# Kernel optimization log

Measured on AMD Instinct MI355X. Metric: run time of the kernel, lower is better.

Reference implementation:

```python
import jax, jax.numpy as jnp
import numpy as np

NH, DK, DV = 8, 10, 10  # num_heads, per-head key dim, per-head value dim (dim_k=dim_v=80)


def setup_inputs() -> dict:
    key = jax.random.key(0)
    k1, k2, k3, k4, k5 = jax.random.split(key, 5)
    B, NX, NY = 64, 512, 512
    x = jax.random.normal(k1, (B, NX, 768), dtype=jnp.float32)
    y = jax.random.normal(k2, (B, NY, 283), dtype=jnp.float32)
    # nn.Linear(bias=False) weights, stored transposed as (in, out); scaled init
    Wq = jax.random.normal(k3, (768, 80), dtype=jnp.float32) * 0.02
    Wk = jax.random.normal(k4, (283, 80), dtype=jnp.float32) * 0.02
    Wv = jax.random.normal(k5, (283, 80), dtype=jnp.float32) * 0.02
    return {"x": x, "y": y, "Wq": Wq, "Wk": Wk, "Wv": Wv}


def reference(x, y, Wq, Wk, Wv):
    B, nx, _ = x.shape
    ny = y.shape[1]
    # projections -> split heads: (B, nh, seq, dhead)
    q = (x @ Wq).reshape(B, nx, NH, DK).transpose(0, 2, 1, 3)
    k = (y @ Wk).reshape(B, ny, NH, DK).transpose(0, 2, 1, 3)
    v = (y @ Wv).reshape(B, ny, NH, DV).transpose(0, 2, 1, 3)
    scale = 1.0 / np.sqrt(DK).astype(np.float32)
    dist = jax.nn.softmax(jnp.einsum("bhqd,bhkd->bhqk", q, k) * scale, axis=-1)
    att = q + jnp.einsum("bhqk,bhkd->bhqd", dist, v)  # residual add of q
    att = att.transpose(0, 2, 1, 3).reshape(B, nx, NH * DV)
    # module returns `result` = flattened attention (fc/BN stack is dead code)
    return att.reshape(B, -1)
```

## Files before the change

kernel.cpp:

```cpp
#include <hip/hip_runtime.h>
#include <stdint.h>

typedef unsigned short u16;
typedef unsigned int   u32;
typedef _Float16       f16;

typedef __attribute__((ext_vector_type(2))) _Float16 half2v;
typedef __attribute__((ext_vector_type(4))) _Float16 half4v;
typedef __attribute__((ext_vector_type(8))) _Float16 half8v;
typedef __attribute__((ext_vector_type(4))) float    floatx4;

#define NXS    512
#define NYS    512
#define NHEAD  8
#define DHEAD  10
#define DMODEL 80
#define DXK    768
#define DYK    283
#define DYKP   288

__device__ inline half2v pk2(float x, float y) {
  return __builtin_bit_cast(half2v, __builtin_amdgcn_cvt_pkrtz(x, y));
}
__device__ inline half4v cvt4(float4 v) {
  return __builtin_shufflevector(pk2(v.x, v.y), pk2(v.z, v.w), 0, 1, 2, 3);
}
__device__ inline half4v h4u32(u32 a, u32 b) {
  return __builtin_shufflevector(__builtin_bit_cast(half2v, a),
                                 __builtin_bit_cast(half2v, b), 0, 1, 2, 3);
}

__global__ __launch_bounds__(256) void w_prep(const float* __restrict__ Wq,
                                              const float* __restrict__ Wk,
                                              const float* __restrict__ Wv,
                                              f16* __restrict__ Tq,
                                              f16* __restrict__ Tk,
                                              f16* __restrict__ Tv) {
  const int idx = blockIdx.x * 256 + threadIdx.x;
  if (idx < 80 * 768) {
    const int c = idx / 768, k = idx - c * 768;
    Tq[idx] = (f16)Wq[k * 80 + c];
  }
  if (idx < 80 * 288) {
    const int c = idx / 288, k = idx - c * 288;
    float a = 0.f, b = 0.f;
    if (k < DYK) { a = Wk[k * 80 + c]; b = Wv[k * 80 + c]; }
    Tk[idx] = (f16)a;
    Tv[idx] = (f16)b;
  }
}

__global__ __launch_bounds__(256) void proj(const float* __restrict__ X,
                                            const float* __restrict__ Y,
                                            const f16* __restrict__ Wtq,
                                            const f16* __restrict__ Wtk,
                                            const f16* __restrict__ Wtv,
                                            f16* __restrict__ Qw,
                                            f16* __restrict__ Kw,
                                            f16* __restrict__ Vw) {
  const int t = threadIdx.x;
  const int wv = t >> 6, lane = t & 63, m16 = lane & 15, quad = lane >> 4;
  const int blk = blockIdx.x;

  if (blk < 512) {
    __shared__ f16 Xs[64 * 40];
    __shared__ f16 Ws[80 * 40];
    const int row0 = blk * 64;
    const int xr_r = t >> 3, xr_k = (t & 7) << 2;
    const int wi0 = t, wi1 = t + 160;

    float4 xr0, xr1;
    uint4 wr0, wr1;
    xr0 = *(const float4*)&X[(size_t)(row0 + xr_r) * DXK + xr_k];
    xr1 = *(const float4*)&X[(size_t)(row0 + xr_r + 32) * DXK + xr_k];
    if (t < 160) {
      wr0 = *(const uint4*)&Wtq[(wi0 >> 2) * DXK + (wi0 & 3) * 8];
      wr1 = *(const uint4*)&Wtq[(wi1 >> 2) * DXK + (wi1 & 3) * 8];
    }

    floatx4 acc[5];
#pragma unroll
    for (int i = 0; i < 5; ++i) acc[i] = (floatx4){0.f, 0.f, 0.f, 0.f};

    for (int s = 0; s < 24; ++s) {
      if (s) __syncthreads();
      *(half4v*)&Xs[xr_r * 40 + xr_k] = cvt4(xr0);
      *(half4v*)&Xs[(xr_r + 32) * 40 + xr_k] = cvt4(xr1);
      if (t < 160) {
        *(uint4*)&Ws[(wi0 >> 2) * 40 + (wi0 & 3) * 8] = wr0;
        *(uint4*)&Ws[(wi1 >> 2) * 40 + (wi1 & 3) * 8] = wr1;
      }
      __syncthreads();
      if (s < 23) {
        const int k0 = (s + 1) * 32;
        xr0 = *(const float4*)&X[(size_t)(row0 + xr_r) * DXK + k0 + xr_k];
        xr1 = *(const float4*)&X[(size_t)(row0 + xr_r + 32) * DXK + k0 + xr_k];
        if (t < 160) {
          wr0 = *(const uint4*)&Wtq[(wi0 >> 2) * DXK + k0 + (wi0 & 3) * 8];
          wr1 = *(const uint4*)&Wtq[(wi1 >> 2) * DXK + k0 + (wi1 & 3) * 8];
        }
      }
      const half8v a = *(const half8v*)&Xs[(wv * 16 + m16) * 40 + quad * 8];
#pragma unroll
      for (int nt = 0; nt < 5; ++nt) {
        const half8v b = *(const half8v*)&Ws[(nt * 16 + m16) * 40 + quad * 8];
        acc[nt] = __builtin_amdgcn_mfma_f32_16x16x32_f16(a, b, acc[nt], 0, 0, 0);
      }
    }
#pragma unroll
    for (int nt = 0; nt < 5; ++nt) {
      const int col = nt * 16 + m16;
#pragma unroll
      for (int p = 0; p < 4; ++p) {
        const int grow = row0 + wv * 16 + quad * 4 + p;
        Qw[(size_t)grow * DMODEL + col] = (f16)acc[nt][p];
      }
    }
  } else {
    __shared__ f16 Ys[64 * 40];
    __shared__ f16 Wks[80 * 40];
    __shared__ f16 Wvs[80 * 40];
    const int row0 = (blk - 512) * 64;
    const int wi0 = t, wi1 = t + 160;

    float yr[8];
    uint4 wk0, wk1, wv0, wv1;
#pragma unroll
    for (int i = 0; i < 8; ++i) {
      const int idx = t + 256 * i;
      const int r = idx >> 5, kk = idx & 31;
      yr[i] = Y[(size_t)(row0 + r) * DYK + kk];
    }
    if (t < 160) {
      wk0 = *(const uint4*)&Wtk[(wi0 >> 2) * DYKP + (wi0 & 3) * 8];
      wk1 = *(const uint4*)&Wtk[(wi1 >> 2) * DYKP + (wi1 & 3) * 8];
      wv0 = *(const uint4*)&Wtv[(wi0 >> 2) * DYKP + (wi0 & 3) * 8];
      wv1 = *(const uint4*)&Wtv[(wi1 >> 2) * DYKP + (wi1 & 3) * 8];
    }

    floatx4 ak[5], av[5];
#pragma unroll
    for (int i = 0; i < 5; ++i) {
      ak[i] = (floatx4){0.f, 0.f, 0.f, 0.f};
      av[i] = (floatx4){0.f, 0.f, 0.f, 0.f};
    }

    for (int s = 0; s < 9; ++s) {
      if (s) __syncthreads();
#pragma unroll
      for (int i = 0; i < 8; ++i) {
        const int idx = t + 256 * i;
        Ys[(idx >> 5) * 40 + (idx & 31)] = (f16)yr[i];
      }
      if (t < 160) {
        *(uint4*)&Wks[(wi0 >> 2) * 40 + (wi0 & 3) * 8] = wk0;
        *(uint4*)&Wks[(wi1 >> 2) * 40 + (wi1 & 3) * 8] = wk1;
        *(uint4*)&Wvs[(wi0 >> 2) * 40 + (wi0 & 3) * 8] = wv0;
        *(uint4*)&Wvs[(wi1 >> 2) * 40 + (wi1 & 3) * 8] = wv1;
      }
      __syncthreads();
      if (s < 8) {
        const int k0 = (s + 1) * 32;
#pragma unroll
        for (int i = 0; i < 8; ++i) {
          const int idx = t + 256 * i;
          const int r = idx >> 5, k = k0 + (idx & 31);
          yr[i] = (k < DYK) ? Y[(size_t)(row0 + r) * DYK + k] : 0.f;
        }
        if (t < 160) {
          wk0 = *(const uint4*)&Wtk[(wi0 >> 2) * DYKP + k0 + (wi0 & 3) * 8];
          wk1 = *(const uint4*)&Wtk[(wi1 >> 2) * DYKP + k0 + (wi1 & 3) * 8];
          wv0 = *(const uint4*)&Wtv[(wi0 >> 2) * DYKP + k0 + (wi0 & 3) * 8];
          wv1 = *(const uint4*)&Wtv[(wi1 >> 2) * DYKP + k0 + (wi1 & 3) * 8];
        }
      }
      const half8v a = *(const half8v*)&Ys[(wv * 16 + m16) * 40 + quad * 8];
#pragma unroll
      for (int nt = 0; nt < 5; ++nt) {
        const half8v bk = *(const half8v*)&Wks[(nt * 16 + m16) * 40 + quad * 8];
        ak[nt] = __builtin_amdgcn_mfma_f32_16x16x32_f16(a, bk, ak[nt], 0, 0, 0);
        const half8v bv = *(const half8v*)&Wvs[(nt * 16 + m16) * 40 + quad * 8];
        av[nt] = __builtin_amdgcn_mfma_f32_16x16x32_f16(a, bv, av[nt], 0, 0, 0);
      }
    }
#pragma unroll
    for (int nt = 0; nt < 5; ++nt) {
      const int col = nt * 16 + m16;
      const int h = col / 10, d = col - h * 10;
#pragma unroll
      for (int p = 0; p < 4; ++p) {
        const int grow = row0 + wv * 16 + quad * 4 + p;
        const int bb = grow >> 9, ny = grow & 511;
        const size_t o = (((size_t)bb * NHEAD + h) * NYS + ny) * DHEAD + d;
        Kw[o] = (f16)ak[nt][p];
        Vw[o] = (f16)av[nt][p];
      }
    }
  }
}

__global__ __launch_bounds__(256) void attn(const f16* __restrict__ Q,
                                            const f16* __restrict__ K,
                                            const f16* __restrict__ V,
                                            float* __restrict__ O) {
  __shared__ f16 Ks[512 * 22];
  __shared__ f16 Vt[16 * 522];
  const int t = threadIdx.x;
  const int wv = t >> 6, lane = t & 63, m16 = lane & 15, quad = lane >> 4;
  const int bh = blockIdx.x >> 1, half = blockIdx.x & 1;
  const int b = bh >> 3, h = bh & 7;

  const u32* Kg = (const u32*)K + (size_t)bh * NYS * 5;
  const u32* Vg = (const u32*)V + (size_t)bh * NYS * 5;
  for (int idx = t; idx < 2560; idx += 256) {
    const u32 row = (u32)idx / 5u, c = (u32)idx - row * 5u;
    const half2v kv = __builtin_bit_cast(half2v, Kg[idx]);
    Ks[row * 22 + 2 * c]     = kv[0];
    Ks[row * 22 + 2 * c + 1] = kv[1];
    const half2v vvv = __builtin_bit_cast(half2v, Vg[idx]);
    Vt[(2 * c) * 522 + row]     = vvv[0];
    Vt[(2 * c + 1) * 522 + row] = vvv[1];
  }
  for (int idx = t; idx < 3072; idx += 256) {
    const u32 row = (u32)idx / 6u, d = 10u + ((u32)idx - row * 6u);
    Ks[row * 22 + d] = (f16)0.f;
  }
  for (int idx = t; idx < 6 * 522; idx += 256)
    Vt[10 * 522 + idx] = (f16)0.f;
  __syncthreads();

  const float scale = 0.31622776601683794f;
#pragma unroll 1
  for (int i = 0; i < 4; ++i) {
    const int qt = half * 16 + wv * 4 + i;
    const int qrow = qt * 16 + m16;
    const u32* Qg32 = (const u32*)(Q + ((size_t)b * NXS + qrow) * DMODEL + h * DHEAD);
    float s0 = 0.f, s1 = 0.f, s2 = 0.f, s3 = 0.f;
    if (quad < 2) {
      const u32 ua = Qg32[quad * 2], ub = Qg32[quad * 2 + 1];
      const half2v ha = __builtin_bit_cast(half2v, ua);
      const half2v hb = __builtin_bit_cast(half2v, ub);
      s0 = (float)ha[0]; s1 = (float)ha[1]; s2 = (float)hb[0]; s3 = (float)hb[1];
    } else if (quad == 2) {
      const u32 ua = Qg32[4];
      const half2v ha = __builtin_bit_cast(half2v, ua);
      s0 = (float)ha[0]; s1 = (float)ha[1];
    }
    const half4v qf = __builtin_shufflevector(pk2(s0 * scale, s1 * scale),
                                              pk2(s2 * scale, s3 * scale),
                                              0, 1, 2, 3);
    floatx4 o0 = (floatx4){0.f, 0.f, 0.f, 0.f};
    floatx4 o1 = (floatx4){0.f, 0.f, 0.f, 0.f};
    float l0 = 0.f, l1 = 0.f;
    for (int kt = 0; kt < 32; kt += 2) {
#pragma unroll
      for (int u = 0; u < 2; ++u) {
        const int ktu = kt + u;
        const int kb = (ktu * 16 + m16) * 22 + quad * 4;
        const half4v kf = h4u32(*(const u32*)&Ks[kb], *(const u32*)&Ks[kb + 2]);
        const floatx4 s = __builtin_amdgcn_mfma_f32_16x16x16f16(
            kf, qf, (floatx4){0.f, 0.f, 0.f, 0.f}, 0, 0, 0);
        const float p0 = __expf(s[0]);
        const float p1 = __expf(s[1]);
        const float p2 = __expf(s[2]);
        const float p3 = __expf(s[3]);
        const half4v pf = __builtin_shufflevector(pk2(p0, p1), pk2(p2, p3),
                                                  0, 1, 2, 3);
        const int vb = m16 * 522 + ktu * 16 + quad * 4;
        const half4v vf = h4u32(*(const u32*)&Vt[vb], *(const u32*)&Vt[vb + 2]);
        if (u == 0) {
          l0 += (p0 + p1) + (p2 + p3);
          o0 = __builtin_amdgcn_mfma_f32_16x16x16f16(pf, vf, o0, 0, 0, 0);
        } else {
          l1 += (p0 + p1) + (p2 + p3);
          o1 = __builtin_amdgcn_mfma_f32_16x16x16f16(pf, vf, o1, 0, 0, 0);
        }
      }
    }
    float lp = l0 + l1;
    lp += __shfl_xor(lp, 16);
    lp += __shfl_xor(lp, 32);
#pragma unroll
    for (int p = 0; p < 4; ++p) {
      const int rq = qt * 16 + quad * 4 + p;
      const float lr = __shfl(lp, quad * 4 + p);
      if (m16 < DHEAD) {
        const float qres = (float)Q[((size_t)b * NXS + rq) * DMODEL + h * DHEAD + m16];
        O[((size_t)b * NXS + rq) * DMODEL + h * DHEAD + m16] =
            qres + (o0[p] + o1[p]) / lr;
      }
    }
  }
}

extern "C" void kernel_launch(void* const* d_in, const int* in_sizes, int n_in,
                              void* d_out, int out_size, void* d_ws, size_t ws_size,
                              hipStream_t stream) {
  const float* x  = (const float*)d_in[0];
  const float* y  = (const float*)d_in[1];
  const float* Wq = (const float*)d_in[2];
  const float* Wk = (const float*)d_in[3];
  const float* Wv = (const float*)d_in[4];
  float* out = (float*)d_out;

  char* ws = (char*)d_ws;
  f16* Wtq = (f16*)(ws);
  f16* Wtk = (f16*)(ws + 122880);
  f16* Wtv = (f16*)(ws + 168960);
  f16* Qw  = (f16*)(ws + 262144);
  f16* Kw  = (f16*)(ws + 5505024);
  f16* Vw  = (f16*)(ws + 10747904);

  w_prep<<<240, 256, 0, stream>>>(Wq, Wk, Wv, Wtq, Wtk, Wtv);
  proj  <<<1024, 256, 0, stream>>>(x, y, Wtq, Wtk, Wtv, Qw, Kw, Vw);
  attn  <<<1024, 256, 0, stream>>>(Qw, Kw, Vw, out);
}
```

Baseline: 239.0 us.

## Load projection MFMA operands directly from global memory, dropping LDS staging

Result: slower. 280.4 us (+17.3%).

```diff
diff --git a/kernel.cpp b/kernel.cpp
--- a/kernel.cpp
+++ b/kernel.cpp
@@ -24,6 +24,10 @@
 }
 __device__ inline half4v cvt4(float4 v) {
   return __builtin_shufflevector(pk2(v.x, v.y), pk2(v.z, v.w), 0, 1, 2, 3);
+}
+__device__ inline half8v cvt8(float4 a, float4 b) {
+  const half4v lo = cvt4(a), hi = cvt4(b);
+  return __builtin_shufflevector(lo, hi, 0, 1, 2, 3, 4, 5, 6, 7);
 }
 __device__ inline half4v h4u32(u32 a, u32 b) {
   return __builtin_shufflevector(__builtin_bit_cast(half2v, a),
@@ -50,63 +54,42 @@
   }
 }
 
-__global__ __launch_bounds__(256) void proj(const float* __restrict__ X,
-                                            const float* __restrict__ Y,
-                                            const f16* __restrict__ Wtq,
-                                            const f16* __restrict__ Wtk,
-                                            const f16* __restrict__ Wtv,
-                                            f16* __restrict__ Qw,
-                                            f16* __restrict__ Kw,
-                                            f16* __restrict__ Vw) {
+__global__ __launch_bounds__(256, 4) void proj(const float* __restrict__ X,
+                                               const float* __restrict__ Y,
+                                               const f16* __restrict__ Wtq,
+                                               const f16* __restrict__ Wtk,
+                                               const f16* __restrict__ Wtv,
+                                               f16* __restrict__ Qw,
+                                               f16* __restrict__ Kw,
+                                               f16* __restrict__ Vw) {
   const int t = threadIdx.x;
   const int wv = t >> 6, lane = t & 63, m16 = lane & 15, quad = lane >> 4;
   const int blk = blockIdx.x;
-
-  if (blk < 512) {
-    __shared__ f16 Xs[64 * 40];
-    __shared__ f16 Ws[80 * 40];
-    const int row0 = blk * 64;
-    const int xr_r = t >> 3, xr_k = (t & 7) << 2;
-    const int wi0 = t, wi1 = t + 160;
-
-    float4 xr0, xr1;
-    uint4 wr0, wr1;
-    xr0 = *(const float4*)&X[(size_t)(row0 + xr_r) * DXK + xr_k];
-    xr1 = *(const float4*)&X[(size_t)(row0 + xr_r + 32) * DXK + xr_k];
-    if (t < 160) {
-      wr0 = *(const uint4*)&Wtq[(wi0 >> 2) * DXK + (wi0 & 3) * 8];
-      wr1 = *(const uint4*)&Wtq[(wi1 >> 2) * DXK + (wi1 & 3) * 8];
-    }
+  const int tile = blk >> 1;
+  const int row0 = tile * 64;
+  const int row = row0 + wv * 16 + m16;
+  const int kq = quad * 8;
+
+  if (!(blk & 1)) {
+    const float* xrow = X + (size_t)row * DXK + kq;
+    const f16*   wqb  = Wtq + m16 * DXK + kq;
 
     floatx4 acc[5];
 #pragma unroll
     for (int i = 0; i < 5; ++i) acc[i] = (floatx4){0.f, 0.f, 0.f, 0.f};
 
+#pragma unroll
     for (int s = 0; s < 24; ++s) {
-      if (s) __syncthreads();
-      *(half4v*)&Xs[xr_r * 40 + xr_k] = cvt4(xr0);
-      *(half4v*)&Xs[(xr_r + 32) * 40 + xr_k] = cvt4(xr1);
-      if (t < 160) {
-        *(uint4*)&Ws[(wi0 >> 2) * 40 + (wi0 & 3) * 8] = wr0;
-        *(uint4*)&Ws[(wi1 >> 2) * 40 + (wi1 & 3) * 8] = wr1;
-      }
-      __syncthreads();
-      if (s < 23) {
-        const int k0 = (s + 1) * 32;
-        xr0 = *(const float4*)&X[(size_t)(row0 + xr_r) * DXK + k0 + xr_k];
-        xr1 = *(const float4*)&X[(size_t)(row0 + xr_r + 32) * DXK + k0 + xr_k];
-        if (t < 160) {
-          wr0 = *(const uint4*)&Wtq[(wi0 >> 2) * DXK + k0 + (wi0 & 3) * 8];
-          wr1 = *(const uint4*)&Wtq[(wi1 >> 2) * DXK + k0 + (wi1 & 3) * 8];
-        }
-      }
-      const half8v a = *(const half8v*)&Xs[(wv * 16 + m16) * 40 + quad * 8];
+      const float4 xa = *(const float4*)(xrow + s * 32);
+      const float4 xb = *(const float4*)(xrow + s * 32 + 4);
+      const half8v a = cvt8(xa, xb);
 #pragma unroll
       for (int nt = 0; nt < 5; ++nt) {
-        const half8v b = *(const half8v*)&Ws[(nt * 16 + m16) * 40 + quad * 8];
+        const half8v b = *(const half8v*)(wqb + nt * 16 * DXK + s * 32);
         acc[nt] = __builtin_amdgcn_mfma_f32_16x16x32_f16(a, b, acc[nt], 0, 0, 0);
       }
     }
+
 #pragma unroll
     for (int nt = 0; nt < 5; ++nt) {
       const int col = nt * 16 + m16;
@@ -117,26 +100,9 @@
       }
     }
   } else {
-    __shared__ f16 Ys[64 * 40];
-    __shared__ f16 Wks[80 * 40];
-    __shared__ f16 Wvs[80 * 40];
-    const int row0 = (blk - 512) * 64;
-    const int wi0 = t, wi1 = t + 160;
-
-    float yr[8];
-    uint4 wk0, wk1, wv0, wv1;
-#pragma unroll
-    for (int i = 0; i < 8; ++i) {
-      const int idx = t + 256 * i;
-      const int r = idx >> 5, kk = idx & 31;
-      yr[i] = Y[(size_t)(row0 + r) * DYK + kk];
-    }
-    if (t < 160) {
-      wk0 = *(const uint4*)&Wtk[(wi0 >> 2) * DYKP + (wi0 & 3) * 8];
-      wk1 = *(const uint4*)&Wtk[(wi1 >> 2) * DYKP + (wi1 & 3) * 8];
-      wv0 = *(const uint4*)&Wtv[(wi0 >> 2) * DYKP + (wi0 & 3) * 8];
-      wv1 = *(const uint4*)&Wtv[(wi1 >> 2) * DYKP + (wi1 & 3) * 8];
-    }
+    const float* yrow = Y + (size_t)row * DYK;
+    const f16*   wkb  = Wtk + m16 * DYKP + kq;
+    const f16*   wvb  = Wtv + m16 * DYKP + kq;
 
     floatx4 ak[5], av[5];
 #pragma unroll
@@ -145,44 +111,25 @@
       av[i] = (floatx4){0.f, 0.f, 0.f, 0.f};
     }
 
+#pragma unroll
     for (int s = 0; s < 9; ++s) {
-      if (s) __syncthreads();
-#pragma unroll
-      for (int i = 0; i < 8; ++i) {
-        const int idx = t + 256 * i;
-        Ys[(idx >> 5) * 40 + (idx & 31)] = (f16)yr[i];
-      }
-      if (t < 160) {
-        *(uint4*)&Wks[(wi0 >> 2) * 40 + (wi0 & 3) * 8] = wk0;
-        *(uint4*)&Wks[(wi1 >> 2) * 40 + (wi1 & 3) * 8] = wk1;
-        *(uint4*)&Wvs[(wi0 >> 2) * 40 + (wi0 & 3) * 8] = wv0;
-        *(uint4*)&Wvs[(wi1 >> 2) * 40 + (wi1 & 3) * 8] = wv1;
-      }
-      __syncthreads();
-      if (s < 8) {
-        const int k0 = (s + 1) * 32;
-#pragma unroll
-        for (int i = 0; i < 8; ++i) {
-          const int idx = t + 256 * i;
-          const int r = idx >> 5, k = k0 + (idx & 31);
-          yr[i] = (k < DYK) ? Y[(size_t)(row0 + r) * DYK + k] : 0.f;
-        }
-        if (t < 160) {
-          wk0 = *(const uint4*)&Wtk[(wi0 >> 2) * DYKP + k0 + (wi0 & 3) * 8];
-          wk1 = *(const uint4*)&Wtk[(wi1 >> 2) * DYKP + k0 + (wi1 & 3) * 8];
-          wv0 = *(const uint4*)&Wtv[(wi0 >> 2) * DYKP + k0 + (wi0 & 3) * 8];
-          wv1 = *(const uint4*)&Wtv[(wi1 >> 2) * DYKP + k0 + (wi1 & 3) * 8];
-        }
-      }
-      const half8v a = *(const half8v*)&Ys[(wv * 16 + m16) * 40 + quad * 8];
+      const int k0 = s * 32 + kq;
+      float yr[8];
+#pragma unroll
+      for (int j = 0; j < 8; ++j)
+        yr[j] = (k0 + j < DYK) ? yrow[k0 + j] : 0.f;
+      half8v a;
+#pragma unroll
+      for (int j = 0; j < 8; ++j) a[j] = (f16)yr[j];
 #pragma unroll
       for (int nt = 0; nt < 5; ++nt) {
-        const half8v bk = *(const half8v*)&Wks[(nt * 16 + m16) * 40 + quad * 8];
+        const half8v bk = *(const half8v*)(wkb + nt * 16 * DYKP + s * 32);
         ak[nt] = __builtin_amdgcn_mfma_f32_16x16x32_f16(a, bk, ak[nt], 0, 0, 0);
-        const half8v bv = *(const half8v*)&Wvs[(nt * 16 + m16) * 40 + quad * 8];
+        const half8v bv = *(const half8v*)(wvb + nt * 16 * DYKP + s * 32);
         av[nt] = __builtin_amdgcn_mfma_f32_16x16x32_f16(a, bv, av[nt], 0, 0, 0);
       }
     }
+
 #pragma unroll
     for (int nt = 0; nt < 5; ++nt) {
       const int col = nt * 16 + m16;
```

## Split attention over four blocks per head, shrink LDS tiles, interleave projection blocks

Applied to the files above, without the earlier changes.

New measurement: 255.9 us. 7.1% more time.

```diff
diff --git a/kernel.cpp b/kernel.cpp
--- a/kernel.cpp
+++ b/kernel.cpp
@@ -61,11 +61,11 @@
   const int t = threadIdx.x;
   const int wv = t >> 6, lane = t & 63, m16 = lane & 15, quad = lane >> 4;
   const int blk = blockIdx.x;
-
-  if (blk < 512) {
+  const int row0 = (blk >> 1) * 64;
+
+  if (!(blk & 1)) {
     __shared__ f16 Xs[64 * 40];
     __shared__ f16 Ws[80 * 40];
-    const int row0 = blk * 64;
     const int xr_r = t >> 3, xr_k = (t & 7) << 2;
     const int wi0 = t, wi1 = t + 160;
 
@@ -120,7 +120,6 @@
     __shared__ f16 Ys[64 * 40];
     __shared__ f16 Wks[80 * 40];
     __shared__ f16 Wvs[80 * 40];
-    const int row0 = (blk - 512) * 64;
     const int wi0 = t, wi1 = t + 160;
 
     float yr[8];
@@ -199,15 +198,18 @@
   }
 }
 
+#define KSTR 20
+#define VSTR 522
+
 __global__ __launch_bounds__(256) void attn(const f16* __restrict__ Q,
                                             const f16* __restrict__ K,
                                             const f16* __restrict__ V,
                                             float* __restrict__ O) {
-  __shared__ f16 Ks[512 * 22];
-  __shared__ f16 Vt[16 * 522];
+  __shared__ f16 Ks[512 * KSTR];
+  __shared__ f16 Vt[10 * VSTR];
   const int t = threadIdx.x;
   const int wv = t >> 6, lane = t & 63, m16 = lane & 15, quad = lane >> 4;
-  const int bh = blockIdx.x >> 1, half = blockIdx.x & 1;
+  const int bh = blockIdx.x >> 2, quarter = blockIdx.x & 3;
   const int b = bh >> 3, h = bh & 7;
 
   const u32* Kg = (const u32*)K + (size_t)bh * NYS * 5;
@@ -215,24 +217,23 @@
   for (int idx = t; idx < 2560; idx += 256) {
     const u32 row = (u32)idx / 5u, c = (u32)idx - row * 5u;
     const half2v kv = __builtin_bit_cast(half2v, Kg[idx]);
-    Ks[row * 22 + 2 * c]     = kv[0];
-    Ks[row * 22 + 2 * c + 1] = kv[1];
+    Ks[row * KSTR + 2 * c]     = kv[0];
+    Ks[row * KSTR + 2 * c + 1] = kv[1];
     const half2v vvv = __builtin_bit_cast(half2v, Vg[idx]);
-    Vt[(2 * c) * 522 + row]     = vvv[0];
-    Vt[(2 * c + 1) * 522 + row] = vvv[1];
+    Vt[(2 * c) * VSTR + row]     = vvv[0];
+    Vt[(2 * c + 1) * VSTR + row] = vvv[1];
   }
   for (int idx = t; idx < 3072; idx += 256) {
     const u32 row = (u32)idx / 6u, d = 10u + ((u32)idx - row * 6u);
-    Ks[row * 22 + d] = (f16)0.f;
-  }
-  for (int idx = t; idx < 6 * 522; idx += 256)
-    Vt[10 * 522 + idx] = (f16)0.f;
+    Ks[row * KSTR + d] = (f16)0.f;
+  }
   __syncthreads();
 
+  const int vrow = (m16 < DHEAD) ? m16 : (m16 - DHEAD);
   const float scale = 0.31622776601683794f;
 #pragma unroll 1
-  for (int i = 0; i < 4; ++i) {
-    const int qt = half * 16 + wv * 4 + i;
+  for (int i = 0; i < 2; ++i) {
+    const int qt = quarter * 8 + wv * 2 + i;
     const int qrow = qt * 16 + m16;
     const u32* Qg32 = (const u32*)(Q + ((size_t)b * NXS + qrow) * DMODEL + h * DHEAD);
     float s0 = 0.f, s1 = 0.f, s2 = 0.f, s3 = 0.f;
@@ -256,7 +257,7 @@
 #pragma unroll
       for (int u = 0; u < 2; ++u) {
         const int ktu = kt + u;
-        const int kb = (ktu * 16 + m16) * 22 + quad * 4;
+        const int kb = (ktu * 16 + m16) * KSTR + quad * 4;
         const half4v kf = h4u32(*(const u32*)&Ks[kb], *(const u32*)&Ks[kb + 2]);
         const floatx4 s = __builtin_amdgcn_mfma_f32_16x16x16f16(
             kf, qf, (floatx4){0.f, 0.f, 0.f, 0.f}, 0, 0, 0);
@@ -266,7 +267,7 @@
         const float p3 = __expf(s[3]);
         const half4v pf = __builtin_shufflevector(pk2(p0, p1), pk2(p2, p3),
                                                   0, 1, 2, 3);
-        const int vb = m16 * 522 + ktu * 16 + quad * 4;
+        const int vb = vrow * VSTR + ktu * 16 + quad * 4;
         const half4v vf = h4u32(*(const u32*)&Vt[vb], *(const u32*)&Vt[vb + 2]);
         if (u == 0) {
           l0 += (p0 + p1) + (p2 + p3);
@@ -313,5 +314,5 @@
 
   w_prep<<<240, 256, 0, stream>>>(Wq, Wk, Wv, Wtq, Wtk, Wtv);
   proj  <<<1024, 256, 0, stream>>>(x, y, Wtq, Wtk, Wtv, Qw, Kw, Vw);
-  attn  <<<1024, 256, 0, stream>>>(Qw, Kw, Vw, out);
-}
+  attn  <<<2048, 256, 0, stream>>>(Qw, Kw, Vw, out);
+}
```

## Split Q projection K-dimension across two blocks, summing partials in attention

Applied to the files above, without the earlier changes.

Measured after the change: 251.3 us. +5.1%, slower.

```diff
diff --git a/kernel.cpp b/kernel.cpp
--- a/kernel.cpp
+++ b/kernel.cpp
@@ -55,34 +55,38 @@
                                             const f16* __restrict__ Wtq,
                                             const f16* __restrict__ Wtk,
                                             const f16* __restrict__ Wtv,
-                                            f16* __restrict__ Qw,
+                                            float* __restrict__ Qa,
+                                            f16* __restrict__ Qb,
                                             f16* __restrict__ Kw,
                                             f16* __restrict__ Vw) {
+  __shared__ f16 smem[8960];
   const int t = threadIdx.x;
   const int wv = t >> 6, lane = t & 63, m16 = lane & 15, quad = lane >> 4;
   const int blk = blockIdx.x;
 
-  if (blk < 512) {
-    __shared__ f16 Xs[64 * 40];
-    __shared__ f16 Ws[80 * 40];
-    const int row0 = blk * 64;
+  if (blk < 1024) {
+    const int khalf = blk >> 9;
+    const int row0 = (blk & 511) * 64;
+    const int kbase = khalf * 384;
+    f16* const Xs = smem;
+    f16* const Ws = smem + 2560;
     const int xr_r = t >> 3, xr_k = (t & 7) << 2;
     const int wi0 = t, wi1 = t + 160;
 
     float4 xr0, xr1;
     uint4 wr0, wr1;
-    xr0 = *(const float4*)&X[(size_t)(row0 + xr_r) * DXK + xr_k];
-    xr1 = *(const float4*)&X[(size_t)(row0 + xr_r + 32) * DXK + xr_k];
+    xr0 = *(const float4*)&X[(size_t)(row0 + xr_r) * DXK + kbase + xr_k];
+    xr1 = *(const float4*)&X[(size_t)(row0 + xr_r + 32) * DXK + kbase + xr_k];
     if (t < 160) {
-      wr0 = *(const uint4*)&Wtq[(wi0 >> 2) * DXK + (wi0 & 3) * 8];
-      wr1 = *(const uint4*)&Wtq[(wi1 >> 2) * DXK + (wi1 & 3) * 8];
+      wr0 = *(const uint4*)&Wtq[(wi0 >> 2) * DXK + kbase + (wi0 & 3) * 8];
+      wr1 = *(const uint4*)&Wtq[(wi1 >> 2) * DXK + kbase + (wi1 & 3) * 8];
     }
 
     floatx4 acc[5];
 #pragma unroll
     for (int i = 0; i < 5; ++i) acc[i] = (floatx4){0.f, 0.f, 0.f, 0.f};
 
-    for (int s = 0; s < 24; ++s) {
+    for (int s = 0; s < 12; ++s) {
       if (s) __syncthreads();
       *(half4v*)&Xs[xr_r * 40 + xr_k] = cvt4(xr0);
       *(half4v*)&Xs[(xr_r + 32) * 40 + xr_k] = cvt4(xr1);
@@ -91,8 +95,8 @@
         *(uint4*)&Ws[(wi1 >> 2) * 40 + (wi1 & 3) * 8] = wr1;
       }
       __syncthreads();
-      if (s < 23) {
-        const int k0 = (s + 1) * 32;
+      if (s < 11) {
+        const int k0 = kbase + (s + 1) * 32;
         xr0 = *(const float4*)&X[(size_t)(row0 + xr_r) * DXK + k0 + xr_k];
         xr1 = *(const float4*)&X[(size_t)(row0 + xr_r + 32) * DXK + k0 + xr_k];
         if (t < 160) {
@@ -113,14 +117,15 @@
 #pragma unroll
       for (int p = 0; p < 4; ++p) {
         const int grow = row0 + wv * 16 + quad * 4 + p;
-        Qw[(size_t)grow * DMODEL + col] = (f16)acc[nt][p];
+        if (khalf == 0) Qa[(size_t)grow * DMODEL + col] = acc[nt][p];
+        else            Qb[(size_t)grow * DMODEL + col] = (f16)acc[nt][p];
       }
     }
   } else {
-    __shared__ f16 Ys[64 * 40];
-    __shared__ f16 Wks[80 * 40];
-    __shared__ f16 Wvs[80 * 40];
-    const int row0 = (blk - 512) * 64;
+    const int row0 = (blk - 1024) * 64;
+    f16* const Ys  = smem;
+    f16* const Wks = smem + 2560;
+    f16* const Wvs = smem + 5760;
     const int wi0 = t, wi1 = t + 160;
 
     float yr[8];
@@ -199,10 +204,11 @@
   }
 }
 
-__global__ __launch_bounds__(256) void attn(const f16* __restrict__ Q,
+__global__ __launch_bounds__(256) void attn(const float* Qa,
+                                            const f16* __restrict__ Qb,
                                             const f16* __restrict__ K,
                                             const f16* __restrict__ V,
-                                            float* __restrict__ O) {
+                                            float* O) {
   __shared__ f16 Ks[512 * 22];
   __shared__ f16 Vt[16 * 522];
   const int t = threadIdx.x;
@@ -234,17 +240,20 @@
   for (int i = 0; i < 4; ++i) {
     const int qt = half * 16 + wv * 4 + i;
     const int qrow = qt * 16 + m16;
-    const u32* Qg32 = (const u32*)(Q + ((size_t)b * NXS + qrow) * DMODEL + h * DHEAD);
+    const float* qa = Qa + ((size_t)b * NXS + qrow) * DMODEL + h * DHEAD;
+    const u32* qb32 = (const u32*)(Qb + ((size_t)b * NXS + qrow) * DMODEL + h * DHEAD);
     float s0 = 0.f, s1 = 0.f, s2 = 0.f, s3 = 0.f;
     if (quad < 2) {
-      const u32 ua = Qg32[quad * 2], ub = Qg32[quad * 2 + 1];
-      const half2v ha = __builtin_bit_cast(half2v, ua);
-      const half2v hb = __builtin_bit_cast(half2v, ub);
-      s0 = (float)ha[0]; s1 = (float)ha[1]; s2 = (float)hb[0]; s3 = (float)hb[1];
+      const float2 a0 = *(const float2*)(qa + quad * 4);
+      const float2 a1 = *(const float2*)(qa + quad * 4 + 2);
+      const half2v h0 = __builtin_bit_cast(half2v, qb32[quad * 2]);
+      const half2v h1 = __builtin_bit_cast(half2v, qb32[quad * 2 + 1]);
+      s0 = a0.x + (float)h0[0]; s1 = a0.y + (float)h0[1];
+      s2 = a1.x + (float)h1[0]; s3 = a1.y + (float)h1[1];
     } else if (quad == 2) {
-      const u32 ua = Qg32[4];
-      const half2v ha = __builtin_bit_cast(half2v, ua);
-      s0 = (float)ha[0]; s1 = (float)ha[1];
+      const float2 a0 = *(const float2*)(qa + 8);
+      const half2v h0 = __builtin_bit_cast(half2v, qb32[4]);
+      s0 = a0.x + (float)h0[0]; s1 = a0.y + (float)h0[1];
     }
     const half4v qf = __builtin_shufflevector(pk2(s0 * scale, s1 * scale),
                                               pk2(s2 * scale, s3 * scale),
@@ -285,9 +294,9 @@
       const int rq = qt * 16 + quad * 4 + p;
       const float lr = __shfl(lp, quad * 4 + p);
       if (m16 < DHEAD) {
-        const float qres = (float)Q[((size_t)b * NXS + rq) * DMODEL + h * DHEAD + m16];
-        O[((size_t)b * NXS + rq) * DMODEL + h * DHEAD + m16] =
-            qres + (o0[p] + o1[p]) / lr;
+        const size_t qidx = ((size_t)b * NXS + rq) * DMODEL + h * DHEAD + m16;
+        const float qres = Qa[qidx] + (float)Qb[qidx];
+        O[qidx] = qres + (o0[p] + o1[p]) / lr;
       }
     }
   }
@@ -307,11 +316,11 @@
   f16* Wtq = (f16*)(ws);
   f16* Wtk = (f16*)(ws + 122880);
   f16* Wtv = (f16*)(ws + 168960);
-  f16* Qw  = (f16*)(ws + 262144);
+  f16* Qb  = (f16*)(ws + 262144);
   f16* Kw  = (f16*)(ws + 5505024);
   f16* Vw  = (f16*)(ws + 10747904);
 
   w_prep<<<240, 256, 0, stream>>>(Wq, Wk, Wv, Wtq, Wtk, Wtv);
-  proj  <<<1024, 256, 0, stream>>>(x, y, Wtq, Wtk, Wtv, Qw, Kw, Vw);
-  attn  <<<1024, 256, 0, stream>>>(Qw, Kw, Vw, out);
-}
+  proj  <<<1536, 256, 0, stream>>>(x, y, Wtq, Wtk, Wtv, out, Qb, Kw, Vw);
+  attn  <<<1024, 256, 0, stream>>>(out, Qb, Kw, Vw, out);
+}
```
